# Kernel optimization log

Hardware: AMD Instinct MI355X
Metric: run time of the kernel (lower is better)

Reference implementation:

```python
import jax, jax.numpy as jnp
from jax import lax
import numpy as np

B = 512
EPS = 1e-5


def _conv(x, w, b):
    # x: [B,C,H,W], w: [O,I,3,3], stride 1, pad 1 (same spatial)
    y = lax.conv_general_dilated(x, w, window_strides=(1, 1),
                                 padding=[(1, 1), (1, 1)],
                                 dimension_numbers=('NCHW', 'OIHW', 'NCHW'))
    return y + b[None, :, None, None]


def _bn(x, g, b, m, v):
    # eval-mode batchnorm with running stats
    inv = g * lax.rsqrt(v + EPS)
    return x * inv[None, :, None, None] + (b - m * inv)[None, :, None, None]


def _maxpool2(x):
    return lax.reduce_window(x, -jnp.inf, lax.max, (1, 1, 2, 2), (1, 1, 2, 2), 'VALID')


def _block(x, w, b, g, be, m, v):
    return _maxpool2(jax.nn.relu(_bn(_conv(x, w, b), g, be, m, v)))


def setup_inputs() -> dict:
    key = jax.random.key(0)
    ks = jax.random.split(key, 12)
    n = lambda k, s: jax.random.normal(k, s, jnp.float32) * 0.05
    z = lambda s: jnp.zeros(s, jnp.float32)
    o = lambda s: jnp.ones(s, jnp.float32)
    return {
        'x': jax.random.normal(ks[0], (B, 1, 48, 48), jnp.float32),
        'conv1_w': n(ks[1], (256, 1, 3, 3)), 'conv1_b': z((256,)),
        'bn1_g': o((256,)), 'bn1_b': z((256,)), 'bn1_m': z((256,)), 'bn1_v': o((256,)),
        'conv2_w': n(ks[2], (128, 256, 3, 3)), 'conv2_b': z((128,)),
        'bn2_g': o((128,)), 'bn2_b': z((128,)), 'bn2_m': z((128,)), 'bn2_v': o((128,)),
        'conv3_w': n(ks[3], (64, 128, 3, 3)), 'conv3_b': z((64,)),
        'bn3_g': o((64,)), 'bn3_b': z((64,)), 'bn3_m': z((64,)), 'bn3_v': o((64,)),
        'fc1_w': n(ks[4], (512, 2304)), 'fc1_b': z((512,)),
        'fc2_w': n(ks[5], (256, 512)), 'fc2_b': z((256,)),
        'att_w': n(ks[6], (64, 256)), 'att_b': z((64,)),
        'fc3_w': n(ks[7], (7, 64)), 'fc3_b': z((7,)),
    }


def reference(x, conv1_w, conv1_b, bn1_g, bn1_b, bn1_m, bn1_v,
              conv2_w, conv2_b, bn2_g, bn2_b, bn2_m, bn2_v,
              conv3_w, conv3_b, bn3_g, bn3_b, bn3_m, bn3_v,
              fc1_w, fc1_b, fc2_w, fc2_b, att_w, att_b, fc3_w, fc3_b):
    out1 = _block(x, conv1_w, conv1_b, bn1_g, bn1_b, bn1_m, bn1_v)      # [B,256,24,24]
    out2 = _block(out1, conv2_w, conv2_b, bn2_g, bn2_b, bn2_m, bn2_v)   # [B,128,12,12]
    out3 = _block(out2, conv3_w, conv3_b, bn3_g, bn3_b, bn3_m, bn3_v)   # [B,64,6,6]
    b_ = out3.shape[0]
    out4 = out3.reshape(b_, -1)                                          # [B,2304]
    out5 = out4 @ fc1_w.T + fc1_b                                        # [B,512]
    out6 = out5 @ fc2_w.T + fc2_b                                        # [B,256]
    # spatial attention: query projected to channel dim of out3
    q = out6 @ att_w.T + att_b                                           # [B,64]
    scores = jnp.einsum('bchw,bc->bhw', out3, q).reshape(b_, -1)         # [B,36]
    attn = jax.nn.softmax(scores, axis=1).reshape(b_, 6, 6)
    g_mod = jnp.einsum('bchw,bhw->bc', out3, attn)                       # [B,64]
    return g_mod @ fc3_w.T + fc3_b                                       # [B,7]
```

## Files before the change

### kernel.cpp

```cpp
#include <hip/hip_runtime.h>
#include <hip/hip_bf16.h>
#include <math.h>

#define EPS_BN 1e-5f

typedef __bf16 bf16x8 __attribute__((ext_vector_type(8)));
typedef float f32x4 __attribute__((ext_vector_type(4)));
typedef float f32x2 __attribute__((ext_vector_type(2)));

__device__ __forceinline__ void gl2lds16(const void* g, void* l) {
  __builtin_amdgcn_global_load_lds(
      (const __attribute__((address_space(1))) unsigned int*)g,
      (__attribute__((address_space(3))) unsigned int*)l, 16, 0, 0);
}

__global__ __launch_bounds__(256) void k_conv1prep(
    const float* __restrict__ x, const float* __restrict__ w,
    const float* __restrict__ cb, const float* __restrict__ g,
    const float* __restrict__ bb, const float* __restrict__ m,
    const float* __restrict__ v, __hip_bfloat16* __restrict__ out1p,
    __hip_bfloat16* __restrict__ out2p, const float* __restrict__ c2w,
    __hip_bfloat16* __restrict__ wt2, const float* __restrict__ c3w,
    __hip_bfloat16* __restrict__ wt3, const float* __restrict__ attw,
    const float* __restrict__ fc2w, const float* __restrict__ fc1w,
    float* __restrict__ Wet, const float* __restrict__ fc1b,
    const float* __restrict__ fc2b, const float* __restrict__ attb,
    float* __restrict__ be, int nprep) {
  __shared__ float xp[14 * 50];
  const int blk = blockIdx.x;
  const int t = threadIdx.x;
  if (blk < nprep) {
    if (blk < 1152) {
      int idx = blk * 256 + t;
      int icr = idx & 7;
      int lhi = (idx >> 3) & 3;
      int oc = (idx >> 5) & 127;
      int rest = idx >> 12;
      int kb = rest & 7;
      int p = rest >> 3;
      int ic = kb * 32 + lhi * 8 + icr;
      wt2[idx] = __float2bfloat16(c2w[(oc * 256 + ic) * 9 + p]);
    } else if (blk < 1440) {
      int idx = (blk - 1152) * 256 + t;
      int icr = idx & 7;
      int oc = (idx >> 3) & 63;
      int rest = idx >> 9;
      int icg = rest & 15;
      int p = rest >> 4;
      wt3[idx] = __float2bfloat16(c3w[(oc * 128 + icg * 8 + icr) * 9 + p]);
    } else if (blk < 1504) {
      float* w32row = xp;
      const int r = blk - 1440;
      float a0 = 0.f, a1 = 0.f;
      for (int j = 0; j < 256; j++) {
        float aw = attw[r * 256 + j];
        a0 = fmaf(aw, fc2w[j * 512 + t], a0);
        a1 = fmaf(aw, fc2w[j * 512 + t + 256], a1);
      }
      w32row[t] = a0;
      w32row[t + 256] = a1;
      __syncthreads();
      float s[9];
#pragma unroll
      for (int i = 0; i < 9; i++) s[i] = 0.f;
      for (int k = 0; k < 512; k++) {
        float wv = w32row[k];
        const float* fr = fc1w + k * 2304 + t;
#pragma unroll
        for (int i = 0; i < 9; i++) s[i] = fmaf(wv, fr[i * 256], s[i]);
      }
#pragma unroll
      for (int i = 0; i < 9; i++) Wet[(i * 256 + t) * 64 + r] = s[i];
    } else {
      float* t1 = xp;
      float s = fc2b[t];
      for (int k = 0; k < 512; k++) s = fmaf(fc2w[t * 512 + k], fc1b[k], s);
      t1[t] = s;
      __syncthreads();
      if (t < 64) {
        float r = attb[t];
        for (int k = 0; k < 256; k++) r = fmaf(attw[t * 256 + k], t1[k], r);
        be[t] = r;
      }
    }
    return;
  }
  const int bq = blk - nprep;
  const int b = bq >> 2, q = bq & 3;
  __hip_bfloat16* ob = out1p + (size_t)b * (26 * 26 * 256);
  const __hip_bfloat16 z = __float2bfloat16(0.f);
  if (q == 0)
    for (int i = t; i < 26 * 256; i += 256) ob[i] = z;
  if (q == 3)
    for (int i = t; i < 26 * 256; i += 256) ob[25 * 26 * 256 + i] = z;
  for (int i = t; i < 6 * 2 * 256; i += 256) {
    int r = 1 + 6 * q + (i >> 9), side = (i >> 8) & 1, c = i & 255;
    ob[(r * 26 + side * 25) * 256 + c] = z;
  }
  {
    __hip_bfloat16* o2 = out2p + (size_t)b * (14 * 14 * 128);
    if (q == 0)
      for (int i = t; i < 14 * 128; i += 256) o2[i] = z;
    if (q == 1)
      for (int i = t; i < 14 * 128; i += 256) o2[13 * 14 * 128 + i] = z;
    if (q == 2)
      for (int i = t; i < 6 * 2 * 128; i += 256) {
        int r = 1 + (i >> 8), side = (i >> 7) & 1, c = i & 127;
        o2[(r * 14 + side * 13) * 128 + c] = z;
      }
    if (q == 3)
      for (int i = t; i < 6 * 2 * 128; i += 256) {
        int r = 7 + (i >> 8), side = (i >> 7) & 1, c = i & 127;
        o2[(r * 14 + side * 13) * 128 + c] = z;
      }
  }
  for (int i = t; i < 14 * 50; i += 256) xp[i] = 0.f;
  __syncthreads();
  const float* xb = x + (size_t)b * 2304;
  for (int i = t; i < 14 * 48; i += 256) {
    int rr = i / 48, c = i - rr * 48;
    int gr = 12 * q - 1 + rr;
    if (gr >= 0 && gr < 48) xp[rr * 50 + c + 1] = xb[gr * 48 + c];
  }
  __syncthreads();
  float wr[9];
#pragma unroll
  for (int i = 0; i < 9; i++) wr[i] = w[t * 9 + i];
  const float scale = g[t] * rsqrtf(v[t] + EPS_BN);
  const float bias = (cb[t] - m[t]) * scale + bb[t];
#pragma unroll
  for (int ohl = 0; ohl < 6; ohl++) {
    const int r0 = 2 * ohl;
    f32x2 c01[4];
#pragma unroll
    for (int r = 0; r < 4; r++) c01[r] = *(const f32x2*)&xp[(r0 + r) * 50];
#pragma unroll 4
    for (int ow = 0; ow < 24; ow++) {
      f32x2 c23[4];
#pragma unroll
      for (int r = 0; r < 4; r++)
        c23[r] = *(const f32x2*)&xp[(r0 + r) * 50 + 2 * ow + 2];
      f32x2 s2a = 0.f, s2b = 0.f;
#pragma unroll
      for (int r = 0; r < 4; r++) {
        f32x2 p0 = c01[r], p2 = c23[r];
        f32x2 p1 = {p0.y, p2.x};
        if (r <= 2) {
          s2a += p0 * wr[r * 3 + 0];
          s2a += p1 * wr[r * 3 + 1];
          s2a += p2 * wr[r * 3 + 2];
        }
        if (r >= 1) {
          s2b += p0 * wr[(r - 1) * 3 + 0];
          s2b += p1 * wr[(r - 1) * 3 + 1];
          s2b += p2 * wr[(r - 1) * 3 + 2];
        }
      }
      f32x2 b0 = s2a * scale + bias;
      f32x2 b1 = s2b * scale + bias;
      float mx = fmaxf(fmaxf(b0.x, b0.y), fmaxf(b1.x, b1.y));
      ob[((6 * q + ohl + 1) * 26 + (ow + 1)) * 256 + t] =
          __float2bfloat16(fmaxf(mx, 0.f));
#pragma unroll
      for (int r = 0; r < 4; r++) c01[r] = c23[r];
    }
  }
}

__global__ __launch_bounds__(256) void k_mconv2(
    const __hip_bfloat16* __restrict__ in, const __hip_bfloat16* __restrict__ wt,
    const float* __restrict__ cb, const float* __restrict__ gg,
    const float* __restrict__ bbv, const float* __restrict__ bm,
    const float* __restrict__ bv, __hip_bfloat16* __restrict__ outp) {
  constexpr int HW = 24, IC = 256, OC = 128, HP = 26, CP = 26;
  constexpr int MTW = 6;
  constexpr int ROWS = 4;
  constexpr int TILES = 6;
  constexpr int WN = 32;
  constexpr int NF = 2;
  constexpr int NCH = 6 * CP * 8;
  constexpr int NCHP = (NCH + 255) & ~255;
  constexpr int NLD = NCHP / 256;
  constexpr int NSTG = 4;
  constexpr int ABUF = NCHP * 16;
  constexpr int KG = IC / 32;
  constexpr int EPITCH = OC + 1;
  constexpr int EBYTES = 48 * EPITCH * 4;
  constexpr int SMB = (2 * ABUF) > EBYTES ? (2 * ABUF) : EBYTES;
  constexpr int NSTEP = NSTG * 18;
  constexpr int D = 3;
  constexpr int AD = 3;

  __shared__ __align__(16) char smraw[SMB];
  float* se = (float*)smraw;

  const int tid = threadIdx.x;
  const int wn = tid >> 6, ln = tid & 63;
  const int lhi = ln >> 4, llo = ln & 15;

  const int per = gridDim.x >> 3;
  const int xcd = blockIdx.x & 7, sl = blockIdx.x >> 3;
  const int b = xcd * (per / TILES) + sl / TILES;
  const int T = sl % TILES;
  const int h0 = T * ROWS;

  const __hip_bfloat16* inb = in + (size_t)b * HP * HP * IC;

  int srcoff[NLD];
#pragma unroll
  for (int i = 0; i < NLD; i++) {
    int ci = tid + i * 256;
    if (ci >= NCH) ci = NCH - 1;
    int kgslot = ci & 7;
    int rest = ci >> 3;
    int c = rest % CP;
    int r = rest / CP;
    int kg = kgslot ^ (c & 7);
    srcoff[i] = ((h0 + r) * HP + c) * IC + kg * 8;
  }
  int abase[2][3][3];
#pragma unroll
  for (int mt = 0; mt < 3; mt++) {
    int m = mt * 16 + llo;
    int hl = m / HW, wl = m % HW;
    int spb_ = (hl * CP + wl) * 8;
#pragma unroll
    for (int pw = 0; pw < 3; pw++) {
      int a0 = (spb_ + pw * 8 + (lhi ^ ((wl + pw) & 7))) * 16;
      abase[0][mt][pw] = a0;
      abase[1][mt][pw] = a0 ^ 64;
    }
  }
  const __hip_bfloat16* wtb = wt + (wn * WN + llo) * 32 + lhi * 8;

  f32x4 acc[MTW][NF];
  const f32x4 fz = {0.f, 0.f, 0.f, 0.f};
#pragma unroll
  for (int i = 0; i < MTW; i++)
#pragma unroll
    for (int j = 0; j < NF; j++) acc[i][j] = fz;

  auto LDA = [&](int s, int t, bf16x8* dst) {
    const int p = t >> 1, ks = t & 1;
    const int ph = p / 3, pw = p % 3;
    const int boff = ph * 3328 + ((s & 1) ? ABUF : 0);
#pragma unroll
    for (int mt = 0; mt < MTW; mt++) {
      dst[mt] = *(const bf16x8*)(smraw + abase[ks][mt % 3][pw] + boff +
                                 (mt >= 3 ? 6656 : 0));
    }
  };

#pragma unroll
  for (int i = 0; i < NLD; i++)
    gl2lds16(inb + srcoff[i], smraw + (tid + i * 256) * 16);
  bf16x8 bq[D][NF];
#pragma unroll
  for (int d = 0; d < D; d++) {
    const int sg = d / 18, pg = (d % 18) >> 1, kf = d & 1;
#pragma unroll
    for (int j = 0; j < NF; j++)
      bq[d][j] = *(const bf16x8*)(wtb +
                                  (size_t)((pg * KG + sg * 2 + kf) * OC) * 32 +
                                  j * 512);
  }
  __syncthreads();

#pragma unroll
  for (int s = 0; s < NSTG; s++) {
    bf16x8 aq[AD][MTW];
    LDA(s, 0, aq[0]);
    LDA(s, 1, aq[1]);
#pragma unroll
    for (int t = 0; t < 18; t++) {
      const int g = s * 18 + t;
      if (t + 2 < 18) LDA(s, t + 2, aq[(t + 2) % AD]);
      __builtin_amdgcn_s_setprio(1);
#pragma unroll
      for (int mt = 0; mt < MTW; mt++)
#pragma unroll
        for (int j = 0; j < NF; j++)
          acc[mt][j] = __builtin_amdgcn_mfma_f32_16x16x32_bf16(
              aq[t % AD][mt], bq[g % D][j], acc[mt][j], 0, 0, 0);
      __builtin_amdgcn_s_setprio(0);
      if (g + D < NSTEP) {
        const int gf = g + D;
        const int sg = gf / 18, pg = (gf % 18) >> 1, kf = gf & 1;
#pragma unroll
        for (int j = 0; j < NF; j++)
          bq[gf % D][j] =
              *(const bf16x8*)(wtb +
                               (size_t)((pg * KG + sg * 2 + kf) * OC) * 32 +
                               j * 512);
      }
      if (t == 13 && s + 1 < NSTG) {
        char* nb = smraw + ((s + 1) & 1) * ABUF;
#pragma unroll
        for (int i = 0; i < NLD; i++)
          gl2lds16(inb + srcoff[i] + (s + 1) * 64, nb + (tid + i * 256) * 16);
      }
    }
    __syncthreads();
  }

  constexpr int OHW = HW / 2;
  constexpr int NP = 1 * OHW * OC;
#pragma unroll
  for (int pz = 0; pz < 2; pz++) {
    if (pz) __syncthreads();
#pragma unroll
    for (int j = 0; j < NF; j++) {
      int n = wn * WN + j * 16 + llo;
      float scale = gg[n] * rsqrtf(bv[n] + EPS_BN);
      float bias = (cb[n] - bm[n]) * scale + bbv[n];
#pragma unroll
      for (int mtl = 0; mtl < 3; mtl++)
#pragma unroll
        for (int r = 0; r < 4; r++) {
          int mrow = mtl * 16 + lhi * 4 + r;
          se[mrow * EPITCH + n] =
              fmaxf(acc[pz * 3 + mtl][j][r] * scale + bias, 0.f);
        }
    }
    __syncthreads();
    for (int sI = tid; sI < NP; sI += 256) {
      int n = sI % OC;
      int ow = (sI / OC) % OHW;
      int mloc = 2 * ow;
      float x0 = se[mloc * EPITCH + n];
      float x1 = se[(mloc + 1) * EPITCH + n];
      float x2 = se[(mloc + HW) * EPITCH + n];
      float x3 = se[(mloc + HW + 1) * EPITCH + n];
      float mx = fmaxf(fmaxf(x0, x1), fmaxf(x2, x3));
      int oh = (h0 >> 1) + pz;
      outp[(((size_t)b * 14 + oh + 1) * 14 + ow + 1) * OC + n] =
          __float2bfloat16(mx);
    }
  }
}

__global__ __launch_bounds__(256) void k_c3attn(
    const __hip_bfloat16* __restrict__ in, const __hip_bfloat16* __restrict__ wt,
    const float* __restrict__ cb, const float* __restrict__ gg,
    const float* __restrict__ bbv, const float* __restrict__ bm,
    const float* __restrict__ bv, const float* __restrict__ Wet,
    const float* __restrict__ be, const float* __restrict__ w3,
    const float* __restrict__ b3, float* __restrict__ out, int b0) {
  constexpr int HW = 12, IC = 128, OC = 64, HP = 14, CP = 14;
  constexpr int NCH = 14 * CP * 8;
  constexpr int NCHP = (NCH + 255) & ~255;
  constexpr int NLD = NCHP / 256;
  constexpr int NSTG = 2;
  constexpr int ABUF = NCHP * 16;
  constexpr int ICG = 16;
  constexpr int EPITCH = OC + 1;

  __shared__ __align__(16) char smraw[2 * ABUF];
  __shared__ float act[64 * 37];
  __shared__ float qp[4][64];
  __shared__ float ql[64], gm[64], sc[36];
  float* se = (float*)smraw;

  const int tid = threadIdx.x;
  const int wv = tid >> 6, ln = tid & 63;
  const int lhi = ln >> 4, llo = ln & 15;
  const int b = blockIdx.x;

  const __hip_bfloat16* inb = in + (size_t)b * HP * HP * IC;

  int srcoff[NLD];
#pragma unroll
  for (int i = 0; i < NLD; i++) {
    int ci = tid + i * 256;
    if (ci >= NCH) ci = NCH - 1;
    int kgslot = ci & 7;
    int rest = ci >> 3;
    int c = rest % CP;
    int r = rest / CP;
    int kg = kgslot ^ (c & 7);
    srcoff[i] = (r * HP + c) * IC + kg * 8;
  }
  int spb[9], wlv[9];
#pragma unroll
  for (int mt = 0; mt < 9; mt++) {
    int m = mt * 16 + llo;
    int hl = m / HW, wl = m % HW;
    spb[mt] = (hl * CP + wl) * 8;
    wlv[mt] = wl;
  }
  const __hip_bfloat16* wtb = wt + (size_t)(lhi * OC + wv * 16 + llo) * 8;

  f32x4 acc[9];
  const f32x4 fz = {0.f, 0.f, 0.f, 0.f};
#pragma unroll
  for (int i = 0; i < 9; i++) acc[i] = fz;

#pragma unroll
  for (int i = 0; i < NLD; i++)
    gl2lds16(inb + srcoff[i], smraw + (tid + i * 256) * 16);
  __syncthreads();

#pragma unroll
  for (int s = 0; s < NSTG; s++) {
    if (s + 1 < NSTG) {
      char* nb = smraw + ((s + 1) & 1) * ABUF;
#pragma unroll
      for (int i = 0; i < NLD; i++)
        gl2lds16(inb + srcoff[i] + (s + 1) * 64, nb + (tid + i * 256) * 16);
    }
    const char* cw = smraw + (s & 1) * ABUF;
#pragma unroll
    for (int tt = 0; tt < 18; tt++) {
      const int p = tt >> 1, ks = tt & 1;
      const int ph = p / 3, pw = p % 3;
      const int kg = ks * 4 + lhi;
      bf16x8 bf =
          *(const bf16x8*)(wtb + ((size_t)(p * ICG + s * 8 + ks * 4) * OC) * 8);
#pragma unroll
      for (int mt = 0; mt < 9; mt++) {
        int slot = spb[mt] + (ph * CP + pw) * 8 + (kg ^ ((wlv[mt] + pw) & 7));
        bf16x8 af = *(const bf16x8*)(cw + slot * 16);
        acc[mt] = __builtin_amdgcn_mfma_f32_16x16x32_bf16(af, bf, acc[mt], 0,
                                                          0, 0);
      }
    }
    __syncthreads();
  }

  {
    const int n = wv * 16 + llo;
    const float scale = gg[n] * rsqrtf(bv[n] + EPS_BN);
    const float bias = (cb[n] - bm[n]) * scale + bbv[n];
#pragma unroll
    for (int pz = 0; pz < 3; pz++) {
      if (pz) __syncthreads();
#pragma unroll
      for (int mtl = 0; mtl < 3; mtl++)
#pragma unroll
        for (int r = 0; r < 4; r++) {
          int mrow = mtl * 16 + lhi * 4 + r;
          se[mrow * EPITCH + n] =
              fmaxf(acc[pz * 3 + mtl][r] * scale + bias, 0.f);
        }
      __syncthreads();
      for (int sI = tid; sI < 2 * 6 * 64; sI += 256) {
        int nn = sI % 64;
        int ow = (sI / 64) % 6;
        int ohl = sI / (64 * 6);
        int mloc = (2 * ohl) * HW + 2 * ow;
        float x0 = se[mloc * EPITCH + nn];
        float x1 = se[(mloc + 1) * EPITCH + nn];
        float x2 = se[(mloc + HW) * EPITCH + nn];
        float x3 = se[(mloc + HW + 1) * EPITCH + nn];
        float mx = fmaxf(fmaxf(x0, x1), fmaxf(x2, x3));
        act[nn * 37 + (pz * 2 + ohl) * 6 + ow] = mx;
      }
    }
  }
  __syncthreads();

  {
    float qpv = 0.f;
    const int n = ln;
#pragma unroll 2
    for (int c2 = wv * 16; c2 < wv * 16 + 16; c2++)
      for (int hw = 0; hw < 36; hw++)
        qpv = fmaf(act[c2 * 37 + hw], Wet[(c2 * 36 + hw) * 64 + n], qpv);
    qp[wv][n] = qpv;
  }
  __syncthreads();
  if (tid < 64)
    ql[tid] = be[tid] + qp[0][tid] + qp[1][tid] + qp[2][tid] + qp[3][tid];
  __syncthreads();
  if (wv == 0) {
    float s = -INFINITY;
    if (ln < 36) {
      float a = 0.f;
      for (int c = 0; c < 64; c++) a = fmaf(act[c * 37 + ln], ql[c], a);
      s = a;
    }
    float mx = s;
    for (int off = 32; off >= 1; off >>= 1)
      mx = fmaxf(mx, __shfl_xor(mx, off));
    float e = (ln < 36) ? expf(s - mx) : 0.f;
    float sum = e;
    for (int off = 32; off >= 1; off >>= 1) sum += __shfl_xor(sum, off);
    if (ln < 36) sc[ln] = e / sum;
  }
  __syncthreads();
  if (wv == 0) {
    float gv = 0.f;
    for (int hw = 0; hw < 36; hw++) gv = fmaf(act[ln * 37 + hw], sc[hw], gv);
    gm[ln] = gv;
  }
  __syncthreads();
  if (tid < 7) {
    float a = b3[tid];
    for (int c = 0; c < 64; c++) a = fmaf(w3[tid * 64 + c], gm[c], a);
    out[(size_t)(b0 + b) * 7 + tid] = a;
  }
}

extern "C" void kernel_launch(void* const* d_in, const int* in_sizes, int n_in,
                              void* d_out, int out_size, void* d_ws,
                              size_t ws_size, hipStream_t stream) {
  const float* x    = (const float*)d_in[0];
  const float* c1w  = (const float*)d_in[1];
  const float* c1b  = (const float*)d_in[2];
  const float* g1   = (const float*)d_in[3];
  const float* bb1  = (const float*)d_in[4];
  const float* m1   = (const float*)d_in[5];
  const float* v1   = (const float*)d_in[6];
  const float* c2w  = (const float*)d_in[7];
  const float* c2b  = (const float*)d_in[8];
  const float* g2   = (const float*)d_in[9];
  const float* bb2  = (const float*)d_in[10];
  const float* m2   = (const float*)d_in[11];
  const float* v2   = (const float*)d_in[12];
  const float* c3w  = (const float*)d_in[13];
  const float* c3b  = (const float*)d_in[14];
  const float* g3   = (const float*)d_in[15];
  const float* bb3  = (const float*)d_in[16];
  const float* m3   = (const float*)d_in[17];
  const float* v3   = (const float*)d_in[18];
  const float* fc1w = (const float*)d_in[19];
  const float* fc1b = (const float*)d_in[20];
  const float* fc2w = (const float*)d_in[21];
  const float* fc2b = (const float*)d_in[22];
  const float* attw = (const float*)d_in[23];
  const float* attb = (const float*)d_in[24];
  const float* fc3w = (const float*)d_in[25];
  const float* fc3b = (const float*)d_in[26];

  const size_t PER_CHUNK = (173056ULL + 25088ULL) * 2;
  const size_t PERSIST = 589824 + 147456 + 589824 + 256 + 8192;
  int CH = 512;
  while (CH > 8 && (size_t)CH * PER_CHUNK + PERSIST > ws_size) CH >>= 1;
  const int NCHK = 512 / CH;

  char* base = (char*)d_ws;
  size_t off = 0;
  auto alloc = [&](size_t nbytes) -> void* {
    void* p = base + off;
    off = (off + nbytes + 255) & ~(size_t)255;
    return p;
  };
  __hip_bfloat16* out1p = (__hip_bfloat16*)alloc((size_t)CH * 173056 * 2);
  __hip_bfloat16* out2p = (__hip_bfloat16*)alloc((size_t)CH * 25088 * 2);
  __hip_bfloat16* wt2  = (__hip_bfloat16*)alloc(589824);
  __hip_bfloat16* wt3  = (__hip_bfloat16*)alloc(147456);
  float* Wet           = (float*)alloc(589824);
  float* be            = (float*)alloc(256);

  for (int c = 0; c < NCHK; c++) {
    const float* xc = x + (size_t)c * CH * 2304;
    const int nprep = (c == 0) ? 1505 : 0;
    k_conv1prep<<<nprep + CH * 4, 256, 0, stream>>>(
        xc, c1w, c1b, g1, bb1, m1, v1, out1p, out2p, c2w, wt2, c3w, wt3, attw,
        fc2w, fc1w, Wet, fc1b, fc2b, attb, be, nprep);
    k_mconv2<<<CH * 6, 256, 0, stream>>>(out1p, wt2, c2b, g2, bb2, m2, v2,
                                         out2p);
    k_c3attn<<<CH, 256, 0, stream>>>(out2p, wt3, c3b, g3, bb3, m3, v3, Wet, be,
                                     fc3w, fc3b, (float*)d_out, c * CH);
  }
}
```

Before: 378.4 us.

## Compute conv1 with bf16 MFMA using split-precision input and weights, one block per image

```diff
diff --git a/kernel.cpp b/kernel.cpp
--- a/kernel.cpp
+++ b/kernel.cpp
@@ -26,7 +26,7 @@
     float* __restrict__ Wet, const float* __restrict__ fc1b,
     const float* __restrict__ fc2b, const float* __restrict__ attb,
     float* __restrict__ be, int nprep) {
-  __shared__ float xp[14 * 50];
+  __shared__ __align__(16) char shraw[10400];
   const int blk = blockIdx.x;
   const int t = threadIdx.x;
   if (blk < nprep) {
@@ -49,7 +49,7 @@
       int p = rest >> 4;
       wt3[idx] = __float2bfloat16(c3w[(oc * 128 + icg * 8 + icr) * 9 + p]);
     } else if (blk < 1504) {
-      float* w32row = xp;
+      float* w32row = (float*)shraw;
       const int r = blk - 1440;
       float a0 = 0.f, a1 = 0.f;
       for (int j = 0; j < 256; j++) {
@@ -63,6 +63,7 @@
       float s[9];
 #pragma unroll
       for (int i = 0; i < 9; i++) s[i] = 0.f;
+#pragma unroll 2
       for (int k = 0; k < 512; k++) {
         float wv = w32row[k];
         const float* fr = fc1w + k * 2304 + t;
@@ -72,7 +73,7 @@
 #pragma unroll
       for (int i = 0; i < 9; i++) Wet[(i * 256 + t) * 64 + r] = s[i];
     } else {
-      float* t1 = xp;
+      float* t1 = (float*)shraw;
       float s = fc2b[t];
       for (int k = 0; k < 512; k++) s = fmaf(fc2w[t * 512 + k], fc1b[k], s);
       t1[t] = s;
@@ -85,84 +86,123 @@
     }
     return;
   }
-  const int bq = blk - nprep;
-  const int b = bq >> 2, q = bq & 3;
+  const int b = blk - nprep;
+  const int wv = t >> 6, ln = t & 63;
+  const int lg = ln >> 4, lcol = ln & 15;
   __hip_bfloat16* ob = out1p + (size_t)b * (26 * 26 * 256);
-  const __hip_bfloat16 z = __float2bfloat16(0.f);
-  if (q == 0)
-    for (int i = t; i < 26 * 256; i += 256) ob[i] = z;
-  if (q == 3)
-    for (int i = t; i < 26 * 256; i += 256) ob[25 * 26 * 256 + i] = z;
-  for (int i = t; i < 6 * 2 * 256; i += 256) {
-    int r = 1 + 6 * q + (i >> 9), side = (i >> 8) & 1, c = i & 255;
-    ob[(r * 26 + side * 25) * 256 + c] = z;
-  }
+
   {
-    __hip_bfloat16* o2 = out2p + (size_t)b * (14 * 14 * 128);
-    if (q == 0)
-      for (int i = t; i < 14 * 128; i += 256) o2[i] = z;
-    if (q == 1)
-      for (int i = t; i < 14 * 128; i += 256) o2[13 * 14 * 128 + i] = z;
-    if (q == 2)
-      for (int i = t; i < 6 * 2 * 128; i += 256) {
-        int r = 1 + (i >> 8), side = (i >> 7) & 1, c = i & 127;
-        o2[(r * 14 + side * 13) * 128 + c] = z;
-      }
-    if (q == 3)
-      for (int i = t; i < 6 * 2 * 128; i += 256) {
-        int r = 7 + (i >> 8), side = (i >> 7) & 1, c = i & 127;
-        o2[(r * 14 + side * 13) * 128 + c] = z;
-      }
-  }
-  for (int i = t; i < 14 * 50; i += 256) xp[i] = 0.f;
-  __syncthreads();
-  const float* xb = x + (size_t)b * 2304;
-  for (int i = t; i < 14 * 48; i += 256) {
-    int rr = i / 48, c = i - rr * 48;
-    int gr = 12 * q - 1 + rr;
-    if (gr >= 0 && gr < 48) xp[rr * 50 + c + 1] = xb[gr * 48 + c];
-  }
-  __syncthreads();
-  float wr[9];
-#pragma unroll
-  for (int i = 0; i < 9; i++) wr[i] = w[t * 9 + i];
-  const float scale = g[t] * rsqrtf(v[t] + EPS_BN);
-  const float bias = (cb[t] - m[t]) * scale + bb[t];
-#pragma unroll
-  for (int ohl = 0; ohl < 6; ohl++) {
-    const int r0 = 2 * ohl;
-    f32x2 c01[4];
-#pragma unroll
-    for (int r = 0; r < 4; r++) c01[r] = *(const f32x2*)&xp[(r0 + r) * 50];
-#pragma unroll 4
-    for (int ow = 0; ow < 24; ow++) {
-      f32x2 c23[4];
-#pragma unroll
-      for (int r = 0; r < 4; r++)
-        c23[r] = *(const f32x2*)&xp[(r0 + r) * 50 + 2 * ow + 2];
-      f32x2 s2a = 0.f, s2b = 0.f;
-#pragma unroll
-      for (int r = 0; r < 4; r++) {
-        f32x2 p0 = c01[r], p2 = c23[r];
-        f32x2 p1 = {p0.y, p2.x};
-        if (r <= 2) {
-          s2a += p0 * wr[r * 3 + 0];
-          s2a += p1 * wr[r * 3 + 1];
-          s2a += p2 * wr[r * 3 + 2];
-        }
-        if (r >= 1) {
-          s2b += p0 * wr[(r - 1) * 3 + 0];
-          s2b += p1 * wr[(r - 1) * 3 + 1];
-          s2b += p2 * wr[(r - 1) * 3 + 2];
-        }
-      }
-      f32x2 b0 = s2a * scale + bias;
-      f32x2 b1 = s2b * scale + bias;
-      float mx = fmaxf(fmaxf(b0.x, b0.y), fmaxf(b1.x, b1.y));
-      ob[((6 * q + ohl + 1) * 26 + (ow + 1)) * 256 + t] =
-          __float2bfloat16(fmaxf(mx, 0.f));
-#pragma unroll
-      for (int r = 0; r < 4; r++) c01[r] = c23[r];
+    unsigned int* p1 = (unsigned int*)ob;
+    for (int i = t; i < 2 * 26 * 128; i += 256) {
+      int side = i / (26 * 128), k = i % (26 * 128);
+      p1[side * 25 * 26 * 128 + k] = 0u;
+    }
+    for (int i = t; i < 24 * 2 * 128; i += 256) {
+      int r = 1 + (i >> 8), side = (i >> 7) & 1, k = i & 127;
+      p1[(r * 26 + side * 25) * 128 + k] = 0u;
+    }
+    unsigned int* p2 = (unsigned int*)(out2p + (size_t)b * (14 * 14 * 128));
+    for (int i = t; i < 2 * 14 * 64; i += 256) {
+      int side = i / (14 * 64), k = i % (14 * 64);
+      p2[side * 13 * 14 * 64 + k] = 0u;
+    }
+    for (int i = t; i < 12 * 2 * 64; i += 256) {
+      int r = 1 + (i >> 7), side = (i >> 6) & 1, k = i & 63;
+      p2[(r * 14 + side * 13) * 64 + k] = 0u;
+    }
+  }
+
+  {
+    unsigned int* zp = (unsigned int*)shraw;
+    for (int i = t; i < 2600; i += 256) zp[i] = 0u;
+  }
+  __syncthreads();
+  {
+    __hip_bfloat16* hp = (__hip_bfloat16*)shraw;
+    const float* xb = x + (size_t)b * 2304;
+    for (int i = t; i < 2304; i += 256) {
+      int r = i / 48, c = i - r * 48;
+      float vv = xb[i];
+      __hip_bfloat16 h = __float2bfloat16(vv);
+      float hv = __bfloat162float(h);
+      hp[(r + 1) * 52 + c + 1] = h;
+      hp[2600 + (r + 1) * 52 + c + 1] = __float2bfloat16(vv - hv);
+    }
+  }
+
+  int toff[8];
+#pragma unroll
+  for (int j = 0; j < 8; j++) {
+    int k = lg * 8 + j;
+    int tap, pl;
+    if (k < 9) {
+      tap = k; pl = 0;
+    } else if (k < 18) {
+      tap = k - 9; pl = 1;
+    } else if (k < 27) {
+      tap = k - 18; pl = 0;
+    } else {
+      tap = 0; pl = 0;
+    }
+    int dy = tap / 3, dx = tap - dy * 3;
+    toff[j] = pl * 2600 + (dy - 1) * 52 + (dx - 1);
+  }
+  bf16x8 bw[4];
+  float scl[4], bia[4];
+#pragma unroll
+  for (int j = 0; j < 4; j++) {
+    int oc = wv * 64 + j * 16 + lcol;
+#pragma unroll
+    for (int jj = 0; jj < 8; jj++) {
+      int k = lg * 8 + jj;
+      __hip_bfloat16 outv = __float2bfloat16(0.f);
+      if (k < 27) {
+        int tap = (k < 9) ? k : (k < 18 ? k - 9 : k - 18);
+        float wv2 = w[oc * 9 + tap];
+        __hip_bfloat16 h = __float2bfloat16(wv2);
+        outv = (k < 18) ? h : __float2bfloat16(wv2 - __bfloat162float(h));
+      }
+      bw[j][jj] = (__bf16)outv;
+    }
+    scl[j] = g[oc] * rsqrtf(v[oc] + EPS_BN);
+    bia[j] = (cb[oc] - m[oc]) * scl[j] + bb[oc];
+  }
+  __syncthreads();
+
+  const __bf16* lp = (const __bf16*)shraw;
+  const f32x4 fz = {0.f, 0.f, 0.f, 0.f};
+  for (int rp = 0; rp < 24; rp++) {
+    const int y0 = rp * 2;
+    __hip_bfloat16* orow = ob + (size_t)(rp + 1) * 26 * 256;
+#pragma unroll
+    for (int mtc = 0; mtc < 3; mtc++) {
+      const int xq = mtc * 16 + lcol;
+      const int bT = (y0 + 1) * 52 + xq + 1;
+      bf16x8 at, ab;
+#pragma unroll
+      for (int j = 0; j < 8; j++) at[j] = lp[bT + toff[j]];
+#pragma unroll
+      for (int j = 0; j < 8; j++) ab[j] = lp[bT + 52 + toff[j]];
+      f32x4 ct[4], cbt[4];
+#pragma unroll
+      for (int j = 0; j < 4; j++) {
+        ct[j] = __builtin_amdgcn_mfma_f32_16x16x32_bf16(at, bw[j], fz, 0, 0, 0);
+        cbt[j] =
+            __builtin_amdgcn_mfma_f32_16x16x32_bf16(ab, bw[j], fz, 0, 0, 0);
+      }
+      const int ow0 = mtc * 8 + lg * 2;
+#pragma unroll
+      for (int j = 0; j < 4; j++) {
+        float p0 =
+            fmaxf(fmaxf(ct[j][0], ct[j][1]), fmaxf(cbt[j][0], cbt[j][1]));
+        float p1 =
+            fmaxf(fmaxf(ct[j][2], ct[j][3]), fmaxf(cbt[j][2], cbt[j][3]));
+        p0 = fmaxf(fmaf(p0, scl[j], bia[j]), 0.f);
+        p1 = fmaxf(fmaf(p1, scl[j], bia[j]), 0.f);
+        int oc = wv * 64 + j * 16 + lcol;
+        orow[(ow0 + 1) * 256 + oc] = __float2bfloat16(p0);
+        orow[(ow0 + 2) * 256 + oc] = __float2bfloat16(p1);
+      }
     }
   }
 }
@@ -555,7 +595,7 @@
   for (int c = 0; c < NCHK; c++) {
     const float* xc = x + (size_t)c * CH * 2304;
     const int nprep = (c == 0) ? 1505 : 0;
-    k_conv1prep<<<nprep + CH * 4, 256, 0, stream>>>(
+    k_conv1prep<<<nprep + CH, 256, 0, stream>>>(
         xc, c1w, c1b, g1, bb1, m1, v1, out1p, out2p, c2w, wt2, c3w, wt3, attw,
         fc2w, fc1w, Wet, fc1b, fc2b, attb, be, nprep);
     k_mconv2<<<CH * 6, 256, 0, stream>>>(out1p, wt2, c2b, g2, bb2, m2, v2,
```

Result: slower. 435.5 us (+15.1%).
